# Kernel tuning notes

Hardware: AMD Instinct MI355X
Metric: run time of the kernel (lower is better)

The kernel has to match this reference:

```python
import jax, jax.numpy as jnp
import numpy as np

# Fixed-point precision used by the MPC framework (fractional bits).
FRAC_BITS = 16
SCALE = float(2 ** FRAC_BITS)

def quantize(v):
    """Snap a real value to the fixed-point grid with f fractional bits
    (models SharedPair fixedpoint / dup_with_precision truncation)."""
    return jnp.round(v * SCALE) / SCALE

def setup_inputs() -> dict:
    key = jax.random.key(0)
    k1, k2 = jax.random.split(key)
    B, D_in, D_out = 8192, 1024, 1024
    x = jax.random.normal(k1, (B, D_in), dtype=jnp.float32)
    # weight init: normal(scale=1/sqrt(D_in+1)) as in the module
    w = jax.random.normal(k2, (D_in, D_out), dtype=jnp.float32) * np.float32(1.0 / np.sqrt(D_in + 1))
    b = jnp.zeros((D_out,), dtype=jnp.float32)
    # inputs/params live on the fixed-point grid in the MPC protocol
    return {"x": quantize(x), "w": quantize(w), "b": b}

def reference(x, w, b):
    # BilinearTriangle.compute_u(x, w) with f_xy = a @ b is a Beaver-triple
    # secure matmul; its plaintext semantics is exactly x @ w (result at
    # doubled fixed-point precision 2f).
    y = x @ w + b  # b is dup_with_precision'ed to y.fixedpoint; same value
    # drelu_binary(y): secure comparison producing the sign bit s = (y > 0)
    s = (y > 0).astype(y.dtype)
    out = y * s  # relu(y, s)
    # dup_with_precision(x[0].fixedpoint): truncate back to f fractional bits
    return quantize(out)
```

## Files before the change

kernel.cpp:

```cpp
#include <hip/hip_runtime.h>
#include <hip/hip_bf16.h>
#include <stdint.h>


typedef __attribute__((ext_vector_type(8))) short short8;
typedef __attribute__((ext_vector_type(4))) float f32x4;
typedef __attribute__((ext_vector_type(4))) unsigned short us4;

__device__ __forceinline__ unsigned short f32_to_bf16_rne(float f) {
    uint32_t u = __float_as_uint(f);
    uint32_t r = u + 0x7FFFu + ((u >> 16) & 1u);
    return (unsigned short)(r >> 16);
}
__device__ __forceinline__ float bf16_to_f32(unsigned short s) {
    return __uint_as_float(((uint32_t)s) << 16);
}

__global__ __launch_bounds__(256) void split_x_kernel(const float* __restrict__ x,
                                                      unsigned short* __restrict__ A2) {
    int i = blockIdx.x * 256 + threadIdx.x;
    float4 v = reinterpret_cast<const float4*>(x)[i];
    int e = i * 4;
    int row = e >> 10;
    int col = e & 1023;
    float vv[4] = {v.x, v.y, v.z, v.w};
    us4 h, m;
    unsigned short* hp = (unsigned short*)&h;
    unsigned short* mp = (unsigned short*)&m;
#pragma unroll
    for (int j = 0; j < 4; ++j) {
        float f = vv[j];
        unsigned short hb = f32_to_bf16_rne(f);
        float r1 = f - bf16_to_f32(hb);
        unsigned short mb = f32_to_bf16_rne(r1);
        hp[j] = hb; mp[j] = mb;
    }
    size_t base = (size_t)row * 2048 + col;
    *reinterpret_cast<us4*>(&A2[base])        = h;
    *reinterpret_cast<us4*>(&A2[base + 1024]) = m;
}

__global__ __launch_bounds__(1024) void split_w_kernel(const float* __restrict__ w,
                                                       unsigned short* __restrict__ Bt2) {
    __shared__ float ts[32][33];
    int tx = threadIdx.x, ty = threadIdx.y;
    int n0 = blockIdx.x * 32, k0 = blockIdx.y * 32;
    ts[ty][tx] = w[(size_t)(k0 + ty) * 1024 + (n0 + tx)];
    __syncthreads();
    float f = ts[tx][ty];
    unsigned short h = f32_to_bf16_rne(f);
    float r = f - bf16_to_f32(h);
    unsigned short l = f32_to_bf16_rne(r);
    int n = n0 + ty, k = k0 + tx;
    Bt2[(size_t)n * 2048 + k]        = h;
    Bt2[(size_t)n * 2048 + 1024 + k] = l;
}

#define BM 256
#define BN 128
#define BK 64
#define NT 48

__device__ __forceinline__ void load16_to_lds(const void* g, void* l) {
    __builtin_amdgcn_global_load_lds(
        (const __attribute__((address_space(1))) unsigned int*)g,
        (__attribute__((address_space(3))) unsigned int*)l,
        16, 0, 0);
}

__global__ __launch_bounds__(512, 2) void gemm_kernel(const unsigned short* __restrict__ A2,
                                                      const unsigned short* __restrict__ Bt2,
                                                      const float* __restrict__ bias,
                                                      float* __restrict__ out) {
    __shared__ unsigned short As[2][BM * BK];
    __shared__ unsigned short Bs[2][BN * BK];

    const int tid  = threadIdx.x;
    const int lane = tid & 63;
    const int wave = tid >> 6;
    const int wr = wave >> 1, wc = wave & 1;

    const int bid = blockIdx.x;
    const int wg  = (bid & 7) * 32 + (bid >> 3);
    const int bm = wg >> 3, bn = wg & 7;
    const int m0 = bm * BM, n0 = bn * BN;

    f32x4 acc[4][4];
#pragma unroll
    for (int i = 0; i < 4; ++i)
#pragma unroll
        for (int j = 0; j < 4; ++j) acc[i][j] = (f32x4)0.0f;

    const int Aseg[3] = {0, 1024, 0};
    const int Bseg[3] = {0, 0, 1024};

    auto stage = [&](int b, int t) {
        const int blk = t >> 4, sub = t & 15;
        const int aoff = Aseg[blk] + sub * 64;
        const int boff = Bseg[blk] + sub * 64;
#pragma unroll
        for (int it = 0; it < 4; ++it) {
            int c = it * 512 + tid;
            int row = c >> 3;
            int sw = (c & 7) ^ (row & 7);
            load16_to_lds(A2 + (size_t)(m0 + row) * 2048 + aoff + sw * 8,
                          (char*)As[b] + c * 16);
        }
#pragma unroll
        for (int it = 0; it < 2; ++it) {
            int c = it * 512 + tid;
            int row = c >> 3;
            int sw = (c & 7) ^ (row & 7);
            load16_to_lds(Bt2 + (size_t)(n0 + row) * 2048 + boff + sw * 8,
                          (char*)Bs[b] + c * 16);
        }
    };

    auto compute = [&](int b) {
#pragma unroll
        for (int kk = 0; kk < 2; ++kk) {
            const int ch = kk * 4 + (lane >> 4);
            short8 af[4], bf[4];
#pragma unroll
            for (int f = 0; f < 4; ++f) {
                int ar = wr * 64 + f * 16 + (lane & 15);
                af[f] = *reinterpret_cast<const short8*>(
                            (const char*)As[b] + ar * 128 + ((ch ^ (ar & 7)) * 16));
                int br = wc * 64 + f * 16 + (lane & 15);
                bf[f] = *reinterpret_cast<const short8*>(
                            (const char*)Bs[b] + br * 128 + ((ch ^ (br & 7)) * 16));
            }
#pragma unroll
            for (int i = 0; i < 4; ++i)
#pragma unroll
                for (int j = 0; j < 4; ++j)
                    acc[i][j] = __builtin_amdgcn_mfma_f32_16x16x32_bf16(af[i], bf[j],
                                                                        acc[i][j], 0, 0, 0);
        }
    };

    stage(0, 0);
    __syncthreads();
    for (int t = 0; t < NT; t += 2) {
        if (t + 1 < NT) stage(1, t + 1);
        compute(0);
        __syncthreads();
        if (t + 2 < NT) stage(0, t + 2);
        compute(1);
        __syncthreads();
    }

    const int colBase = n0 + wc * 64 + (lane & 15);
    const int rowBase = m0 + wr * 64 + ((lane >> 4) << 2);
#pragma unroll
    for (int i = 0; i < 4; ++i) {
#pragma unroll
        for (int j = 0; j < 4; ++j) {
            int col = colBase + j * 16;
            float bv = bias[col];
#pragma unroll
            for (int r = 0; r < 4; ++r) {
                int row = rowBase + i * 16 + r;
                float y = acc[i][j][r] + bv;
                y = fmaxf(y, 0.0f);
                y = rintf(y * 65536.0f) * (1.0f / 65536.0f);
                out[(size_t)row * 1024 + col] = y;
            }
        }
    }
}

__global__ __launch_bounds__(256) void naive_kernel(const float* __restrict__ x,
                                                    const float* __restrict__ w,
                                                    const float* __restrict__ bias,
                                                    float* __restrict__ out) {
    int idx = blockIdx.x * 256 + threadIdx.x;
    int row = idx >> 10, col = idx & 1023;
    float s = bias[col];
    for (int k = 0; k < 1024; ++k)
        s += x[(size_t)row * 1024 + k] * w[(size_t)k * 1024 + col];
    s = fmaxf(s, 0.0f);
    out[idx] = rintf(s * 65536.0f) * (1.0f / 65536.0f);
}

extern "C" void kernel_launch(void* const* d_in, const int* in_sizes, int n_in,
                              void* d_out, int out_size, void* d_ws, size_t ws_size,
                              hipStream_t stream) {
    const float* x = (const float*)d_in[0];
    const float* w = (const float*)d_in[1];
    const float* b = (const float*)d_in[2];
    float* out = (float*)d_out;

    const size_t needA = (size_t)8192 * 2048 * 2;
    const size_t needB = (size_t)1024 * 2048 * 2;
    if (ws_size < needA + needB) {
        naive_kernel<<<(8192 * 1024) / 256, 256, 0, stream>>>(x, w, b, out);
        return;
    }
    unsigned short* A2  = (unsigned short*)d_ws;
    unsigned short* Bt2 = (unsigned short*)((char*)d_ws + needA);

    split_x_kernel<<<(8192 * 1024 / 4) / 256, 256, 0, stream>>>(x, A2);
    split_w_kernel<<<dim3(32, 32), dim3(32, 32), 0, stream>>>(w, Bt2);
    gemm_kernel<<<256, 512, 0, stream>>>(A2, Bt2, b, out);
}
```

Measured before the change: 146.8 us.

## Triple-buffer GEMM LDS pipeline with interleaved staging and priority-boosted MFMA phases

The GEMM main loop moves from a double-buffered stage/compute pattern with full __syncthreads to a triple-buffered pipeline that prefetches two tiles ahead. Global-to-LDS loads are split into small chunks interleaved between four MFMA sub-phases, using explicit vmcnt/lgkmcnt waits, s_barrier and s_setprio so memory traffic overlaps matrix math and load latency is hidden. It also widens split_x to handle 8 elements per thread for larger vector loads and stores. The cost is more LDS (about 144KB per block, which rules out two blocks per CU) and a fragile hand-written wait-count schedule.

```diff
diff --git a/kernel.cpp b/kernel.cpp
--- a/kernel.cpp
+++ b/kernel.cpp
@@ -6,6 +6,7 @@
 typedef __attribute__((ext_vector_type(8))) short short8;
 typedef __attribute__((ext_vector_type(4))) float f32x4;
 typedef __attribute__((ext_vector_type(4))) unsigned short us4;
+typedef __attribute__((ext_vector_type(8))) unsigned short us8;
 
 __device__ __forceinline__ unsigned short f32_to_bf16_rne(float f) {
     uint32_t u = __float_as_uint(f);
@@ -19,16 +20,17 @@
 __global__ __launch_bounds__(256) void split_x_kernel(const float* __restrict__ x,
                                                       unsigned short* __restrict__ A2) {
     int i = blockIdx.x * 256 + threadIdx.x;
-    float4 v = reinterpret_cast<const float4*>(x)[i];
-    int e = i * 4;
+    int e = i * 8;
     int row = e >> 10;
     int col = e & 1023;
-    float vv[4] = {v.x, v.y, v.z, v.w};
-    us4 h, m;
+    float4 v0 = reinterpret_cast<const float4*>(x)[2 * i];
+    float4 v1 = reinterpret_cast<const float4*>(x)[2 * i + 1];
+    float vv[8] = {v0.x, v0.y, v0.z, v0.w, v1.x, v1.y, v1.z, v1.w};
+    us8 h, m;
     unsigned short* hp = (unsigned short*)&h;
     unsigned short* mp = (unsigned short*)&m;
 #pragma unroll
-    for (int j = 0; j < 4; ++j) {
+    for (int j = 0; j < 8; ++j) {
         float f = vv[j];
         unsigned short hb = f32_to_bf16_rne(f);
         float r1 = f - bf16_to_f32(hb);
@@ -36,8 +38,8 @@
         hp[j] = hb; mp[j] = mb;
     }
     size_t base = (size_t)row * 2048 + col;
-    *reinterpret_cast<us4*>(&A2[base])        = h;
-    *reinterpret_cast<us4*>(&A2[base + 1024]) = m;
+    *reinterpret_cast<us8*>(&A2[base])        = h;
+    *reinterpret_cast<us8*>(&A2[base + 1024]) = m;
 }
 
 __global__ __launch_bounds__(1024) void split_w_kernel(const float* __restrict__ w,
@@ -72,8 +74,8 @@
                                                       const unsigned short* __restrict__ Bt2,
                                                       const float* __restrict__ bias,
                                                       float* __restrict__ out) {
-    __shared__ unsigned short As[2][BM * BK];
-    __shared__ unsigned short Bs[2][BN * BK];
+    __shared__ unsigned short As[3][BM * BK];
+    __shared__ unsigned short Bs[3][BN * BK];
 
     const int tid  = threadIdx.x;
     const int lane = tid & 63;
@@ -91,64 +93,145 @@
 #pragma unroll
         for (int j = 0; j < 4; ++j) acc[i][j] = (f32x4)0.0f;
 
-    const int Aseg[3] = {0, 1024, 0};
-    const int Bseg[3] = {0, 0, 1024};
-
-    auto stage = [&](int b, int t) {
-        const int blk = t >> 4, sub = t & 15;
-        const int aoff = Aseg[blk] + sub * 64;
-        const int boff = Bseg[blk] + sub * 64;
-#pragma unroll
-        for (int it = 0; it < 4; ++it) {
-            int c = it * 512 + tid;
-            int row = c >> 3;
-            int sw = (c & 7) ^ (row & 7);
-            load16_to_lds(A2 + (size_t)(m0 + row) * 2048 + aoff + sw * 8,
-                          (char*)As[b] + c * 16);
-        }
-#pragma unroll
-        for (int it = 0; it < 2; ++it) {
-            int c = it * 512 + tid;
-            int row = c >> 3;
-            int sw = (c & 7) ^ (row & 7);
-            load16_to_lds(Bt2 + (size_t)(n0 + row) * 2048 + boff + sw * 8,
-                          (char*)Bs[b] + c * 16);
-        }
+    auto aoff_of = [&](int t) { int blk = t >> 4; return ((blk == 1) ? 1024 : 0) + (t & 15) * 64; };
+    auto boff_of = [&](int t) { int blk = t >> 4; return ((blk == 2) ? 1024 : 0) + (t & 15) * 64; };
+
+    auto stageA = [&](int b, int aoff, int it) {
+        int c = it * 512 + tid;
+        int row = c >> 3;
+        int sw = (c & 7) ^ (row & 7);
+        load16_to_lds(A2 + (size_t)(m0 + row) * 2048 + aoff + sw * 8,
+                      (char*)As[b] + c * 16);
     };
-
-    auto compute = [&](int b) {
-#pragma unroll
-        for (int kk = 0; kk < 2; ++kk) {
-            const int ch = kk * 4 + (lane >> 4);
-            short8 af[4], bf[4];
+    auto stageBf = [&](int b, int boff, int it) {
+        int c = it * 512 + tid;
+        int row = c >> 3;
+        int sw = (c & 7) ^ (row & 7);
+        load16_to_lds(Bt2 + (size_t)(n0 + row) * 2048 + boff + sw * 8,
+                      (char*)Bs[b] + c * 16);
+    };
+
+    auto do_tile = [&](int b, int t, bool doStage, int nb) {
+        const char* Ab = (const char*)As[b];
+        const char* Bb = (const char*)Bs[b];
+        const int aoff2 = aoff_of(t + 2);
+        const int boff2 = boff_of(t + 2);
+        short8 af[4], bf[2];
+        {
+            const int ch = (lane >> 4);
 #pragma unroll
             for (int f = 0; f < 4; ++f) {
                 int ar = wr * 64 + f * 16 + (lane & 15);
-                af[f] = *reinterpret_cast<const short8*>(
-                            (const char*)As[b] + ar * 128 + ((ch ^ (ar & 7)) * 16));
-                int br = wc * 64 + f * 16 + (lane & 15);
-                bf[f] = *reinterpret_cast<const short8*>(
-                            (const char*)Bs[b] + br * 128 + ((ch ^ (br & 7)) * 16));
-            }
-#pragma unroll
-            for (int i = 0; i < 4; ++i)
-#pragma unroll
-                for (int j = 0; j < 4; ++j)
-                    acc[i][j] = __builtin_amdgcn_mfma_f32_16x16x32_bf16(af[i], bf[j],
-                                                                        acc[i][j], 0, 0, 0);
+                af[f] = *reinterpret_cast<const short8*>(Ab + ar * 128 + ((ch ^ (ar & 7)) << 4));
+            }
+#pragma unroll
+            for (int j = 0; j < 2; ++j) {
+                int br = wc * 64 + j * 16 + (lane & 15);
+                bf[j] = *reinterpret_cast<const short8*>(Bb + br * 128 + ((ch ^ (br & 7)) << 4));
+            }
+            if (doStage) { stageA(nb, aoff2, 0); stageA(nb, aoff2, 1); }
+            __builtin_amdgcn_s_barrier();
+            asm volatile("s_waitcnt lgkmcnt(0)" ::: "memory");
+            __builtin_amdgcn_sched_barrier(0);
+            __builtin_amdgcn_s_setprio(1);
+#pragma unroll
+            for (int i = 0; i < 4; ++i)
+#pragma unroll
+                for (int j = 0; j < 2; ++j)
+                    acc[i][j] = __builtin_amdgcn_mfma_f32_16x16x32_bf16(af[i], bf[j], acc[i][j], 0, 0, 0);
+            __builtin_amdgcn_s_setprio(0);
+            __builtin_amdgcn_s_barrier();
+        }
+        {
+            const int ch = (lane >> 4);
+#pragma unroll
+            for (int j = 0; j < 2; ++j) {
+                int br = wc * 64 + (2 + j) * 16 + (lane & 15);
+                bf[j] = *reinterpret_cast<const short8*>(Bb + br * 128 + ((ch ^ (br & 7)) << 4));
+            }
+            if (doStage) { stageA(nb, aoff2, 2); stageA(nb, aoff2, 3); }
+            __builtin_amdgcn_s_barrier();
+            asm volatile("s_waitcnt lgkmcnt(0)" ::: "memory");
+            __builtin_amdgcn_sched_barrier(0);
+            __builtin_amdgcn_s_setprio(1);
+#pragma unroll
+            for (int i = 0; i < 4; ++i)
+#pragma unroll
+                for (int j = 0; j < 2; ++j)
+                    acc[i][2 + j] = __builtin_amdgcn_mfma_f32_16x16x32_bf16(af[i], bf[j], acc[i][2 + j], 0, 0, 0);
+            __builtin_amdgcn_s_setprio(0);
+            __builtin_amdgcn_s_barrier();
+        }
+        {
+            const int ch = 4 + (lane >> 4);
+#pragma unroll
+            for (int f = 0; f < 4; ++f) {
+                int ar = wr * 64 + f * 16 + (lane & 15);
+                af[f] = *reinterpret_cast<const short8*>(Ab + ar * 128 + ((ch ^ (ar & 7)) << 4));
+            }
+#pragma unroll
+            for (int j = 0; j < 2; ++j) {
+                int br = wc * 64 + j * 16 + (lane & 15);
+                bf[j] = *reinterpret_cast<const short8*>(Bb + br * 128 + ((ch ^ (br & 7)) << 4));
+            }
+            if (doStage) { stageBf(nb, boff2, 0); stageBf(nb, boff2, 1); }
+            __builtin_amdgcn_s_barrier();
+            asm volatile("s_waitcnt lgkmcnt(0)" ::: "memory");
+            __builtin_amdgcn_sched_barrier(0);
+            __builtin_amdgcn_s_setprio(1);
+#pragma unroll
+            for (int i = 0; i < 4; ++i)
+#pragma unroll
+                for (int j = 0; j < 2; ++j)
+                    acc[i][j] = __builtin_amdgcn_mfma_f32_16x16x32_bf16(af[i], bf[j], acc[i][j], 0, 0, 0);
+            __builtin_amdgcn_s_setprio(0);
+            __builtin_amdgcn_s_barrier();
+        }
+        {
+            const int ch = 4 + (lane >> 4);
+#pragma unroll
+            for (int j = 0; j < 2; ++j) {
+                int br = wc * 64 + (2 + j) * 16 + (lane & 15);
+                bf[j] = *reinterpret_cast<const short8*>(Bb + br * 128 + ((ch ^ (br & 7)) << 4));
+            }
+            __builtin_amdgcn_s_barrier();
+            asm volatile("s_waitcnt lgkmcnt(0)" ::: "memory");
+            __builtin_amdgcn_sched_barrier(0);
+            __builtin_amdgcn_s_setprio(1);
+#pragma unroll
+            for (int i = 0; i < 4; ++i)
+#pragma unroll
+                for (int j = 0; j < 2; ++j)
+                    acc[i][2 + j] = __builtin_amdgcn_mfma_f32_16x16x32_bf16(af[i], bf[j], acc[i][2 + j], 0, 0, 0);
+            __builtin_amdgcn_s_setprio(0);
         }
     };
 
-    stage(0, 0);
-    __syncthreads();
-    for (int t = 0; t < NT; t += 2) {
-        if (t + 1 < NT) stage(1, t + 1);
-        compute(0);
-        __syncthreads();
-        if (t + 2 < NT) stage(0, t + 2);
-        compute(1);
-        __syncthreads();
-    }
+#pragma unroll
+    for (int it = 0; it < 4; ++it) stageA(0, aoff_of(0), it);
+#pragma unroll
+    for (int it = 0; it < 2; ++it) stageBf(0, boff_of(0), it);
+#pragma unroll
+    for (int it = 0; it < 4; ++it) stageA(1, aoff_of(1), it);
+#pragma unroll
+    for (int it = 0; it < 2; ++it) stageBf(1, boff_of(1), it);
+    asm volatile("s_waitcnt vmcnt(6)" ::: "memory");
+    __builtin_amdgcn_s_barrier();
+
+    int cur = 0;
+#pragma unroll 1
+    for (int t = 0; t < NT - 2; ++t) {
+        int nb = (cur == 0) ? 2 : cur - 1;
+        do_tile(cur, t, true, nb);
+        asm volatile("s_waitcnt vmcnt(6)" ::: "memory");
+        __builtin_amdgcn_s_barrier();
+        cur = (cur == 2) ? 0 : cur + 1;
+    }
+    do_tile(cur, NT - 2, false, 0);
+    asm volatile("s_waitcnt vmcnt(0)" ::: "memory");
+    __builtin_amdgcn_s_barrier();
+    cur = (cur == 2) ? 0 : cur + 1;
+    do_tile(cur, NT - 1, false, 0);
 
     const int colBase = n0 + wc * 64 + (lane & 15);
     const int rowBase = m0 + wr * 64 + ((lane >> 4) << 2);
@@ -200,7 +283,7 @@
     unsigned short* A2  = (unsigned short*)d_ws;
     unsigned short* Bt2 = (unsigned short*)((char*)d_ws + needA);
 
-    split_x_kernel<<<(8192 * 1024 / 4) / 256, 256, 0, stream>>>(x, A2);
+    split_x_kernel<<<(8192 * 1024 / 8) / 256, 256, 0, stream>>>(x, A2);
     split_w_kernel<<<dim3(32, 32), dim3(32, 32), 0, stream>>>(w, Bt2);
     gemm_kernel<<<256, 512, 0, stream>>>(A2, Bt2, b, out);
 }
```

New measurement: 154.5 us. 5.3% more time.

## Triple-buffer GEMM LDS with fine-grained interleaved prefetch and barriers

Applied to the files above, without the earlier changes.

Replaces the double-buffered GEMM main loop with a three-stage LDS ring. Each tile's global-to-LDS prefetch is split into two halves interleaved between the two MFMA sub-steps, with explicit vmcnt waits, s_barrier and setprio around the MFMA blocks. LDS addresses are also precomputed per thread, and split_x now processes 8 elements per thread. The aim is to hide global load latency and cut full syncthreads stalls. In exchange LDS use rises to 144KB per block, which may limit occupancy with launch_bounds(512,2), and the manual waitcnt logic is fragile.

```diff
diff --git a/kernel.cpp b/kernel.cpp
--- a/kernel.cpp
+++ b/kernel.cpp
@@ -5,7 +5,9 @@
 
 typedef __attribute__((ext_vector_type(8))) short short8;
 typedef __attribute__((ext_vector_type(4))) float f32x4;
-typedef __attribute__((ext_vector_type(4))) unsigned short us4;
+typedef __attribute__((ext_vector_type(8))) unsigned short us8;
+
+template <int N> struct IC { static constexpr int v = N; };
 
 __device__ __forceinline__ unsigned short f32_to_bf16_rne(float f) {
     uint32_t u = __float_as_uint(f);
@@ -19,16 +21,17 @@
 __global__ __launch_bounds__(256) void split_x_kernel(const float* __restrict__ x,
                                                       unsigned short* __restrict__ A2) {
     int i = blockIdx.x * 256 + threadIdx.x;
-    float4 v = reinterpret_cast<const float4*>(x)[i];
-    int e = i * 4;
+    int e = i * 8;
     int row = e >> 10;
     int col = e & 1023;
-    float vv[4] = {v.x, v.y, v.z, v.w};
-    us4 h, m;
+    float4 v0 = reinterpret_cast<const float4*>(x)[2 * i];
+    float4 v1 = reinterpret_cast<const float4*>(x)[2 * i + 1];
+    float vv[8] = {v0.x, v0.y, v0.z, v0.w, v1.x, v1.y, v1.z, v1.w};
+    us8 h, m;
     unsigned short* hp = (unsigned short*)&h;
     unsigned short* mp = (unsigned short*)&m;
 #pragma unroll
-    for (int j = 0; j < 4; ++j) {
+    for (int j = 0; j < 8; ++j) {
         float f = vv[j];
         unsigned short hb = f32_to_bf16_rne(f);
         float r1 = f - bf16_to_f32(hb);
@@ -36,8 +39,8 @@
         hp[j] = hb; mp[j] = mb;
     }
     size_t base = (size_t)row * 2048 + col;
-    *reinterpret_cast<us4*>(&A2[base])        = h;
-    *reinterpret_cast<us4*>(&A2[base + 1024]) = m;
+    *reinterpret_cast<us8*>(&A2[base])        = h;
+    *reinterpret_cast<us8*>(&A2[base + 1024]) = m;
 }
 
 __global__ __launch_bounds__(1024) void split_w_kernel(const float* __restrict__ w,
@@ -68,12 +71,26 @@
         16, 0, 0);
 }
 
+__device__ __forceinline__ void rd4(short8* dst, const void* base, const int* offs) {
+#pragma unroll
+    for (int f = 0; f < 4; ++f)
+        dst[f] = *reinterpret_cast<const short8*>((const char*)base + offs[f]);
+}
+
+__device__ __forceinline__ void mfma16(f32x4 (&acc)[4][4], const short8* af, const short8* bf) {
+#pragma unroll
+    for (int i = 0; i < 4; ++i)
+#pragma unroll
+        for (int j = 0; j < 4; ++j)
+            acc[i][j] = __builtin_amdgcn_mfma_f32_16x16x32_bf16(af[i], bf[j], acc[i][j], 0, 0, 0);
+}
+
 __global__ __launch_bounds__(512, 2) void gemm_kernel(const unsigned short* __restrict__ A2,
                                                       const unsigned short* __restrict__ Bt2,
                                                       const float* __restrict__ bias,
                                                       float* __restrict__ out) {
-    __shared__ unsigned short As[2][BM * BK];
-    __shared__ unsigned short Bs[2][BN * BK];
+    __shared__ unsigned short As[3][BM * BK];
+    __shared__ unsigned short Bs[3][BN * BK];
 
     const int tid  = threadIdx.x;
     const int lane = tid & 63;
@@ -91,64 +108,109 @@
 #pragma unroll
         for (int j = 0; j < 4; ++j) acc[i][j] = (f32x4)0.0f;
 
-    const int Aseg[3] = {0, 1024, 0};
-    const int Bseg[3] = {0, 0, 1024};
-
-    auto stage = [&](int b, int t) {
-        const int blk = t >> 4, sub = t & 15;
-        const int aoff = Aseg[blk] + sub * 64;
-        const int boff = Bseg[blk] + sub * 64;
-#pragma unroll
-        for (int it = 0; it < 4; ++it) {
-            int c = it * 512 + tid;
-            int row = c >> 3;
-            int sw = (c & 7) ^ (row & 7);
-            load16_to_lds(A2 + (size_t)(m0 + row) * 2048 + aoff + sw * 8,
-                          (char*)As[b] + c * 16);
-        }
-#pragma unroll
-        for (int it = 0; it < 2; ++it) {
-            int c = it * 512 + tid;
-            int row = c >> 3;
-            int sw = (c & 7) ^ (row & 7);
-            load16_to_lds(Bt2 + (size_t)(n0 + row) * 2048 + boff + sw * 8,
-                          (char*)Bs[b] + c * 16);
-        }
+    int a0[4], a1[4], b0[4], b1[4];
+    {
+        const int ch0 = lane >> 4, ch1 = 4 + (lane >> 4);
+#pragma unroll
+        for (int f = 0; f < 4; ++f) {
+            int ar = wr * 64 + f * 16 + (lane & 15);
+            a0[f] = ar * 128 + ((ch0 ^ (ar & 7)) << 4);
+            a1[f] = ar * 128 + ((ch1 ^ (ar & 7)) << 4);
+            int br = wc * 64 + f * 16 + (lane & 15);
+            b0[f] = br * 128 + ((ch0 ^ (br & 7)) << 4);
+            b1[f] = br * 128 + ((ch1 ^ (br & 7)) << 4);
+        }
+    }
+    int aTh[4], bTh[2];
+#pragma unroll
+    for (int it = 0; it < 4; ++it) {
+        int c = it * 512 + tid, row = c >> 3, sw = (c & 7) ^ (row & 7);
+        aTh[it] = (m0 + row) * 2048 + sw * 8;
+    }
+#pragma unroll
+    for (int it = 0; it < 2; ++it) {
+        int c = it * 512 + tid, row = c >> 3, sw = (c & 7) ^ (row & 7);
+        bTh[it] = (n0 + row) * 2048 + sw * 8;
+    }
+    const int dst16 = tid * 16;
+
+    auto aoff_of = [](int t) { int blk = t >> 4; return ((blk == 1) ? 1024 : 0) + (t & 15) * 64; };
+    auto boff_of = [](int t) { int blk = t >> 4; return ((blk == 2) ? 1024 : 0) + (t & 15) * 64; };
+
+    auto tile = [&](auto BC, auto NBC, int t, bool doStage) {
+        constexpr int B  = decltype(BC)::v;
+        constexpr int NB = decltype(NBC)::v;
+        short8 af[4], bf[4];
+        rd4(af, As[B], a0);
+        rd4(bf, Bs[B], b0);
+        if (doStage) {
+            const unsigned short* pA_ = A2 + aoff_of(t + 2);
+            load16_to_lds(pA_ + aTh[0], (char*)As[NB] + 0 * 8192 + dst16);
+            load16_to_lds(pA_ + aTh[1], (char*)As[NB] + 1 * 8192 + dst16);
+            load16_to_lds(pA_ + aTh[2], (char*)As[NB] + 2 * 8192 + dst16);
+        }
+        __builtin_amdgcn_s_barrier();
+        __builtin_amdgcn_s_setprio(1);
+        mfma16(acc, af, bf);
+        __builtin_amdgcn_s_setprio(0);
+        __builtin_amdgcn_s_barrier();
+        rd4(af, As[B], a1);
+        rd4(bf, Bs[B], b1);
+        if (doStage) {
+            const unsigned short* pA_ = A2 + aoff_of(t + 2);
+            const unsigned short* pB_ = Bt2 + boff_of(t + 2);
+            load16_to_lds(pA_ + aTh[3], (char*)As[NB] + 3 * 8192 + dst16);
+            load16_to_lds(pB_ + bTh[0], (char*)Bs[NB] + 0 * 8192 + dst16);
+            load16_to_lds(pB_ + bTh[1], (char*)Bs[NB] + 1 * 8192 + dst16);
+        }
+        __builtin_amdgcn_s_barrier();
+        __builtin_amdgcn_s_setprio(1);
+        mfma16(acc, af, bf);
+        __builtin_amdgcn_s_setprio(0);
+        asm volatile("s_waitcnt lgkmcnt(0)" ::: "memory");
     };
 
-    auto compute = [&](int b) {
-#pragma unroll
-        for (int kk = 0; kk < 2; ++kk) {
-            const int ch = kk * 4 + (lane >> 4);
-            short8 af[4], bf[4];
-#pragma unroll
-            for (int f = 0; f < 4; ++f) {
-                int ar = wr * 64 + f * 16 + (lane & 15);
-                af[f] = *reinterpret_cast<const short8*>(
-                            (const char*)As[b] + ar * 128 + ((ch ^ (ar & 7)) * 16));
-                int br = wc * 64 + f * 16 + (lane & 15);
-                bf[f] = *reinterpret_cast<const short8*>(
-                            (const char*)Bs[b] + br * 128 + ((ch ^ (br & 7)) * 16));
-            }
-#pragma unroll
-            for (int i = 0; i < 4; ++i)
-#pragma unroll
-                for (int j = 0; j < 4; ++j)
-                    acc[i][j] = __builtin_amdgcn_mfma_f32_16x16x32_bf16(af[i], bf[j],
-                                                                        acc[i][j], 0, 0, 0);
-        }
-    };
-
-    stage(0, 0);
-    __syncthreads();
-    for (int t = 0; t < NT; t += 2) {
-        if (t + 1 < NT) stage(1, t + 1);
-        compute(0);
-        __syncthreads();
-        if (t + 2 < NT) stage(0, t + 2);
-        compute(1);
-        __syncthreads();
-    }
+    {
+        const unsigned short* pA_ = A2 + aoff_of(0);
+        const unsigned short* pB_ = Bt2 + boff_of(0);
+        load16_to_lds(pA_ + aTh[0], (char*)As[0] + 0 * 8192 + dst16);
+        load16_to_lds(pA_ + aTh[1], (char*)As[0] + 1 * 8192 + dst16);
+        load16_to_lds(pA_ + aTh[2], (char*)As[0] + 2 * 8192 + dst16);
+        load16_to_lds(pA_ + aTh[3], (char*)As[0] + 3 * 8192 + dst16);
+        load16_to_lds(pB_ + bTh[0], (char*)Bs[0] + 0 * 8192 + dst16);
+        load16_to_lds(pB_ + bTh[1], (char*)Bs[0] + 1 * 8192 + dst16);
+        const unsigned short* qA_ = A2 + aoff_of(1);
+        const unsigned short* qB_ = Bt2 + boff_of(1);
+        load16_to_lds(qA_ + aTh[0], (char*)As[1] + 0 * 8192 + dst16);
+        load16_to_lds(qA_ + aTh[1], (char*)As[1] + 1 * 8192 + dst16);
+        load16_to_lds(qA_ + aTh[2], (char*)As[1] + 2 * 8192 + dst16);
+        load16_to_lds(qA_ + aTh[3], (char*)As[1] + 3 * 8192 + dst16);
+        load16_to_lds(qB_ + bTh[0], (char*)Bs[1] + 0 * 8192 + dst16);
+        load16_to_lds(qB_ + bTh[1], (char*)Bs[1] + 1 * 8192 + dst16);
+    }
+    asm volatile("s_waitcnt vmcnt(6)" ::: "memory");
+    __builtin_amdgcn_s_barrier();
+
+#pragma unroll 1
+    for (int tt = 0; tt < 15; ++tt) {
+        const int t = tt * 3;
+        tile(IC<0>{}, IC<2>{}, t, true);
+        asm volatile("s_waitcnt vmcnt(6)" ::: "memory");
+        __builtin_amdgcn_s_barrier();
+        tile(IC<1>{}, IC<0>{}, t + 1, true);
+        asm volatile("s_waitcnt vmcnt(6)" ::: "memory");
+        __builtin_amdgcn_s_barrier();
+        tile(IC<2>{}, IC<1>{}, t + 2, true);
+        asm volatile("s_waitcnt vmcnt(6)" ::: "memory");
+        __builtin_amdgcn_s_barrier();
+    }
+    tile(IC<0>{}, IC<2>{}, 45, true);
+    asm volatile("s_waitcnt vmcnt(6)" ::: "memory");
+    __builtin_amdgcn_s_barrier();
+    tile(IC<1>{}, IC<0>{}, 46, false);
+    asm volatile("s_waitcnt vmcnt(0)" ::: "memory");
+    __builtin_amdgcn_s_barrier();
+    tile(IC<2>{}, IC<0>{}, 47, false);
 
     const int colBase = n0 + wc * 64 + (lane & 15);
     const int rowBase = m0 + wr * 64 + ((lane >> 4) << 2);
@@ -200,7 +262,7 @@
     unsigned short* A2  = (unsigned short*)d_ws;
     unsigned short* Bt2 = (unsigned short*)((char*)d_ws + needA);
 
-    split_x_kernel<<<(8192 * 1024 / 4) / 256, 256, 0, stream>>>(x, A2);
+    split_x_kernel<<<(8192 * 1024 / 8) / 256, 256, 0, stream>>>(x, A2);
     split_w_kernel<<<dim3(32, 32), dim3(32, 32), 0, stream>>>(w, Bt2);
     gemm_kernel<<<256, 512, 0, stream>>>(A2, Bt2, b, out);
 }
```

New measurement: 150.1 us. 2.3% more time.
